# Kernel optimization log

Hardware: AMD Instinct MI355X
Metric: run time of the kernel (lower is better)

The kernel has to match this reference:

```python
import jax, jax.numpy as jnp
import numpy as np

H = 1024; NH = 16; L = 4; K = 128; N = 65536
ADIM_MOVE = 9; ADIM_TURN = 4; S = 2 * K + 2


def setup_inputs() -> dict:
    key = jax.random.key(0)
    ks = jax.random.split(key, 24)
    s = 0.02
    d = {}
    d['x'] = jax.random.normal(ks[0], (1, H), jnp.float32)
    d['memory_vectors'] = jax.random.normal(ks[1], (N, H), jnp.float32)
    d['memory_next_vectors'] = jax.random.normal(ks[2], (N, H), jnp.float32)
    d['memory_surprises'] = jax.random.uniform(ks[3], (N,), jnp.float32)
    d['memory_rewards'] = jax.random.normal(ks[4], (N,), jnp.float32)
    d['rand_noise'] = jax.random.uniform(ks[5], (N,), jnp.float32)
    d['action_idx_move'] = jax.random.randint(ks[6], (N,), 0, ADIM_MOVE)
    d['action_idx_turn'] = jax.random.randint(ks[7], (N,), 0, ADIM_TURN)
    d['start_token'] = jax.random.uniform(ks[8], (1, H)) * 2 - 1
    d['pos_emb'] = jax.random.uniform(ks[9], (S, H)) * 2 - 1
    d['in_proj_w'] = jax.random.normal(ks[10], (L, 3 * H, H)) * s
    d['in_proj_b'] = jnp.zeros((L, 3 * H))
    d['out_w'] = jax.random.normal(ks[11], (L, H, H)) * s
    d['out_b'] = jnp.zeros((L, H))
    d['ln1_w'] = jnp.ones((L, H)); d['ln1_b'] = jnp.zeros((L, H))
    d['ln2_w'] = jnp.ones((L, H)); d['ln2_b'] = jnp.zeros((L, H))
    d['ffn_w1'] = jax.random.normal(ks[12], (L, 4 * H, H)) * s
    d['ffn_b1'] = jnp.zeros((L, 4 * H))
    d['ffn_w2'] = jax.random.normal(ks[13], (L, H, 4 * H)) * s
    d['ffn_b2'] = jnp.zeros((L, H))
    d['act_move_w1'] = jax.random.normal(ks[14], (H, ADIM_MOVE)) * s
    d['act_move_b1'] = jnp.zeros((H,))
    d['act_move_w2'] = jax.random.normal(ks[15], (H, H)) * s
    d['act_move_b2'] = jnp.zeros((H,))
    d['act_turn_w1'] = jax.random.normal(ks[16], (H, ADIM_TURN)) * s
    d['act_turn_b1'] = jnp.zeros((H,))
    d['act_turn_w2'] = jax.random.normal(ks[17], (H, H)) * s
    d['act_turn_b2'] = jnp.zeros((H,))
    d['vh_w1'] = jax.random.normal(ks[18], (4 * H, H)) * s
    d['vh_b1'] = jnp.zeros((4 * H,))
    d['vh_w2'] = jax.random.normal(ks[19], (1, 4 * H)) * s
    d['vh_b2'] = jnp.zeros((1,))
    return d


def _get_scores(v):
    # tie-aware average rank / N (matches torch unique_consecutive logic)
    srt = jnp.sort(v)
    left = jnp.searchsorted(srt, v, side='left')
    right = jnp.searchsorted(srt, v, side='right')
    return ((left + right - 1).astype(v.dtype) / 2) / v.shape[0]


def _ln(x, w, b):
    m = x.mean(-1, keepdims=True)
    var = ((x - m) ** 2).mean(-1, keepdims=True)
    return (x - m) / jnp.sqrt(var + 1e-5) * w + b


def _gelu(x):
    return jax.nn.gelu(x, approximate=False)


def _mha(x, wqkv, bqkv, wo, bo, mask):
    dh = H // NH
    qkv = x @ wqkv.T + bqkv                      # [S, 3H]
    q, k, v = jnp.split(qkv, 3, axis=-1)
    q = q.reshape(-1, NH, dh); k = k.reshape(-1, NH, dh); v = v.reshape(-1, NH, dh)
    att = jnp.einsum('qhd,khd->hqk', q, k) / np.sqrt(dh).astype(np.float32)
    att = jax.nn.softmax(att + mask, axis=-1)
    o = jnp.einsum('hqk,khd->qhd', att, v).reshape(-1, H)
    return o @ wo.T + bo


def reference(x, memory_vectors, memory_next_vectors, memory_surprises, memory_rewards, rand_noise, action_idx_move, action_idx_turn, start_token, pos_emb, in_proj_w, in_proj_b, out_w, out_b, ln1_w, ln1_b, ln2_w, ln2_b, ffn_w1, ffn_b1, ffn_w2, ffn_b2, act_move_w1, act_move_b1, act_move_w2, act_move_b2, act_turn_w1, act_turn_b1, act_turn_w2, act_turn_b2, vh_w1, vh_b1, vh_w2, vh_b2):
    eps = 1e-8
    # ---- scoring (no_grad in original) ----
    xs = jax.lax.stop_gradient(x)
    xn = xs / jnp.maximum(jnp.linalg.norm(xs, axis=-1, keepdims=True), eps)
    mn = memory_vectors / jnp.maximum(jnp.linalg.norm(memory_vectors, axis=-1, keepdims=True), eps)
    sim = mn @ xn[0]                              # [N]
    scores = _get_scores(memory_surprises) ** 2 + _get_scores(sim) ** 2 + _get_scores(rand_noise) ** 2
    _, idx = jax.lax.top_k(scores, K)             # [K]
    # ---- gather memories + action one-hots ----
    sel = jax.lax.stop_gradient(memory_vectors[idx])   # [K, H]
    oh_move = jax.nn.one_hot(action_idx_move[idx], ADIM_MOVE, dtype=x.dtype)
    oh_turn = jax.nn.one_hot(action_idx_turn[idx], ADIM_TURN, dtype=x.dtype)
    av_move = _gelu(oh_move @ act_move_w1.T + act_move_b1) @ act_move_w2.T + act_move_b2
    av_turn = _gelu(oh_turn @ act_turn_w1.T + act_turn_b1) @ act_turn_w2.T + act_turn_b2
    av = (av_move + av_turn) / 2                  # mean over actions
    # interleave [v0, a0, v1, a1, ...], prepend start, append target
    vecs = jnp.stack((sel, av), axis=1).reshape(-1, H)
    vecs = jnp.concatenate((start_token, vecs, x), axis=0)   # [S, H]
    vecs = vecs + pos_emb
    mask = jnp.where(jnp.tril(jnp.ones((S, S), bool)), 0.0, -jnp.inf).astype(x.dtype)
    for l in range(L):
        vecs = vecs + _mha(_ln(vecs, ln1_w[l], ln1_b[l]), in_proj_w[l], in_proj_b[l], out_w[l], out_b[l], mask)
        h = _ln(vecs, ln2_w[l], ln2_b[l])
        vecs = vecs + _gelu(h @ ffn_w1[l].T + ffn_b1[l]) @ ffn_w2[l].T + ffn_b2[l]
    vidx = jnp.arange(K + 1) * 2 + 1
    vh_in = vecs[vidx]
    vp = _gelu(vh_in @ vh_w1.T + vh_b1) @ vh_w2.T + vh_b2   # [K+1, 1]
    sel_rewards = memory_rewards[idx]
    losses = (vp[:-1].ravel() - sel_rewards) ** 2            # mse, reduction='none'
    return (vecs[1:], memory_next_vectors[idx], vp[-1], losses, sel_rewards)
```

## Files before the change

### kernel.cpp

```cpp
#include <hip/hip_runtime.h>
#include <hip/hip_bf16.h>
#include <math.h>
#include <stdint.h>

typedef unsigned int u32;
typedef unsigned short u16;
typedef unsigned long long u64;

#define NM   65536
#define HD   1024
#define KS   128
#define SQ   258
#define NL   4
#define NBIN 65536
#define CCAP 2048

using bf16x8 = __attribute__((ext_vector_type(8))) short;
using f32x4v = __attribute__((ext_vector_type(4))) float;

static constexpr size_t A256(size_t x){ return (x + 255) & ~(size_t)255; }

constexpr size_t OFF_H3   = 0;
constexpr size_t OFF_C3   = OFF_H3 + (size_t)3*NBIN*4;
constexpr size_t OFF_HS   = OFF_C3 + (size_t)3*NBIN*4;
constexpr size_t ZERO_BYTES = OFF_HS + (size_t)NBIN*4;
constexpr u32 ZBLK = 1792;
constexpr size_t OFF_BS   = A256(ZERO_BYTES);
constexpr size_t OFF_P3   = A256(OFF_BS + 192*4);
constexpr size_t OFF_K3   = A256(OFF_P3 + (size_t)3*(NBIN+1)*4);
constexpr size_t OFF_L3   = A256(OFF_K3 + (size_t)3*NM*4);
constexpr size_t OFF_KSC  = A256(OFF_L3 + (size_t)3*NM*2);
constexpr size_t OFF_IDX  = A256(OFF_KSC + (size_t)NM*4);
constexpr size_t OFF_REW  = A256(OFF_IDX  + (size_t)KS*4);
constexpr size_t OFF_HM   = A256(OFF_REW  + (size_t)KS*4);
constexpr size_t OFF_HT   = A256(OFF_HM   + (size_t)KS*HD*2);
constexpr size_t OFF_VECS = A256(OFF_HT   + (size_t)KS*HD*2);
constexpr size_t OFF_LNB  = A256(OFF_VECS + (size_t)SQ*HD*4);
constexpr size_t OFF_QKV  = A256(OFF_LNB  + (size_t)SQ*HD*2);
constexpr size_t OFF_ATT  = A256(OFF_QKV  + (size_t)SQ*3*HD*2);
constexpr size_t OFF_FFH  = A256(OFF_ATT  + (size_t)SQ*HD*2);
constexpr size_t OFF_VHIN = A256(OFF_FFH  + (size_t)SQ*4*HD*2);
constexpr size_t OFF_WB   = A256(OFF_VHIN + (size_t)129*HD*2);
constexpr size_t NWELEM   = 56623104;
constexpr size_t OFF_PART = A256(OFF_WB + NWELEM*2);

constexpr size_t WB_IN = 0;
constexpr size_t WB_O  = WB_IN + (size_t)4*3*HD*HD;
constexpr size_t WB_F1 = WB_O  + (size_t)4*HD*HD;
constexpr size_t WB_F2 = WB_F1 + (size_t)4*4*HD*HD;
constexpr size_t WB_AM = WB_F2 + (size_t)4*4*HD*HD;
constexpr size_t WB_AT = WB_AM + (size_t)HD*HD;
constexpr size_t WB_VH = WB_AT + (size_t)HD*HD;

constexpr int OUT_NEXT = 257*HD;
constexpr int OUT_VP   = OUT_NEXT + KS*HD;
constexpr int OUT_LOSS = OUT_VP + 1;
constexpr int OUT_REWO = OUT_LOSS + KS;

__device__ __forceinline__ float gelu_f(float v){
  return 0.5f*v*(1.0f + erff(v*0.70710678118654752440f));
}

__device__ __forceinline__ u16 f2bf(float f){
  __hip_bfloat16 h = __float2bfloat16(f);
  u16 s; __builtin_memcpy(&s, &h, sizeof(u16));
  return s;
}

__device__ __forceinline__ float bf2f(u16 v){ return __uint_as_float(((u32)v) << 16); }

__device__ __forceinline__ float4 unpk4(u64 pk){
  u32 lo = (u32)pk, hi = (u32)(pk >> 32);
  float4 v;
  v.x = __uint_as_float(lo << 16);
  v.y = __uint_as_float(lo & 0xFFFF0000u);
  v.z = __uint_as_float(hi << 16);
  v.w = __uint_as_float(hi & 0xFFFF0000u);
  return v;
}

__device__ __forceinline__ u64 pk4(float4 v){
  u16 r[4] = { f2bf(v.x), f2bf(v.y), f2bf(v.z), f2bf(v.w) };
  u64 pk; __builtin_memcpy(&pk, r, 8);
  return pk;
}

__device__ __forceinline__ u32 fkey(float v){
  u32 b = __float_as_uint(v);
  return (b >> 31) ? ~b : (b | 0x80000000u);
}

__device__ __forceinline__ void gload16(const u16* g, u16* l){
  __builtin_amdgcn_global_load_lds(
      (const __attribute__((address_space(1))) unsigned int*)g,
      (__attribute__((address_space(3))) unsigned int*)l, 16, 0, 0);
}

struct WSeg { const float* s; u16* d; u32 base4, end4; };
struct WCA { WSeg seg[7]; u32 tot4; u32* z; };
__global__ __launch_bounds__(256) void k_wconv(WCA a){
  if(blockIdx.x < ZBLK) a.z[blockIdx.x*256 + threadIdx.x] = 0u;
  u32 i = blockIdx.x*256 + threadIdx.x;
  if(i >= a.tot4) return;
  #pragma unroll
  for(int j=0;j<7;++j){
    if(i < a.seg[j].end4){
      u32 off = i - a.seg[j].base4;
      float4 v = *(const float4*)&a.seg[j].s[(size_t)off*4];
      *(u64*)&a.seg[j].d[(size_t)off*4] = pk4(v);
      return;
    }
  }
}

__global__ __launch_bounds__(256) void k_simkey(const float* __restrict__ mv, const float* __restrict__ x,
                                                const float* __restrict__ surp, const float* __restrict__ noise,
                                                u32* __restrict__ keys3, u32* __restrict__ hist3){
  __shared__ float xs[HD];
  __shared__ float red[256];
  int t = threadIdx.x;
  float s = 0.f;
  for(int i=t;i<HD;i+=256){ float v=x[i]; s += v*v; }
  red[t]=s; __syncthreads();
  for(int o=128;o>0;o>>=1){ if(t<o) red[t]+=red[t+o]; __syncthreads(); }
  float nrm = fmaxf(sqrtf(red[0]), 1e-8f);
  for(int i=t;i<HD;i+=256) xs[i] = x[i]/nrm;
  __syncthreads();
  int lane = t & 63, w = t >> 6;
  #pragma unroll
  for(int rep=0;rep<2;++rep){
    int row = blockIdx.x*8 + rep*4 + w;
    const float4* p = (const float4*)(mv + (size_t)row*HD);
    const float4* q = (const float4*)xs;
    float d=0.f, ss=0.f;
    #pragma unroll
    for(int r=0;r<4;++r){
      float4 v = p[lane + 64*r]; float4 u = q[lane + 64*r];
      d  += v.x*u.x + v.y*u.y + v.z*u.z + v.w*u.w;
      ss += v.x*v.x + v.y*v.y + v.z*v.z + v.w*v.w;
    }
    for(int off=32;off>0;off>>=1){ d += __shfl_xor(d,off,64); ss += __shfl_xor(ss,off,64); }
    if(lane==0){
      float sim = d / fmaxf(sqrtf(ss),1e-8f);
      float vals[3] = { surp[row], sim, noise[row] };
      #pragma unroll
      for(int a=0;a<3;++a){
        u32 k = fkey(vals[a]);
        keys3[(size_t)a*NM + row] = k;
        atomicAdd(&hist3[(size_t)a*NBIN + (k >> 16)], 1u);
      }
    }
  }
}

__global__ __launch_bounds__(256) void k_scanA(const u32* __restrict__ hist3, u32* __restrict__ bsum){
  __shared__ u32 red[256];
  int blk = blockIdx.x;
  int t = threadIdx.x;
  const u32* h = hist3 + (size_t)(blk>>6)*NBIN + (size_t)(blk&63)*1024;
  u32 s = 0;
  #pragma unroll
  for(int j=0;j<4;++j) s += h[t*4+j];
  red[t]=s; __syncthreads();
  for(int o=128;o>0;o>>=1){ if(t<o) red[t]+=red[t+o]; __syncthreads(); }
  if(t==0) bsum[blk] = red[0];
}

__global__ __launch_bounds__(256) void k_scanC(const u32* __restrict__ hist3, const u32* __restrict__ bsum,
                                               u32* __restrict__ pref3){
  __shared__ u32 part[256];
  int blk = blockIdx.x;
  int t = threadIdx.x;
  int a = blk >> 6, c = blk & 63;
  u32 base = 0;
  for(int j=0;j<c;++j) base += bsum[a*64 + j];
  const u32* h = hist3 + (size_t)a*NBIN + (size_t)c*1024;
  u32* pref = pref3 + (size_t)a*(NBIN+1) + (size_t)c*1024;
  u32 loc[4]; u32 s = 0;
  #pragma unroll
  for(int j=0;j<4;++j){ loc[j] = h[t*4+j]; s += loc[j]; }
  part[t] = s; __syncthreads();
  for(int off=1;off<256;off<<=1){
    u32 u = (t >= off) ? part[t-off] : 0u;
    __syncthreads(); part[t] += u; __syncthreads();
  }
  u32 run = base + part[t] - s;
  #pragma unroll
  for(int j=0;j<4;++j){ pref[t*4+j] = run; run += loc[j]; }
  if(c == 63 && t == 255) pref3[(size_t)a*(NBIN+1) + NBIN] = NM;
}

__global__ void k_scatter3(const u32* __restrict__ keys3, const u32* __restrict__ pref3,
                           u32* __restrict__ cnt3, u16* __restrict__ lo3){
  int i = blockIdx.x*256 + threadIdx.x;
  if(i >= NM) return;
  #pragma unroll
  for(int a=0;a<3;++a){
    u32 k = keys3[(size_t)a*NM + i];
    u32 b = k >> 16;
    u32 pos = pref3[(size_t)a*(NBIN+1) + b] + atomicAdd(&cnt3[(size_t)a*NBIN + b], 1u);
    lo3[(size_t)a*NM + pos] = (u16)(k & 0xFFFFu);
  }
}

__global__ void k_rank3score(const u32* __restrict__ keys3, const u32* __restrict__ pref3,
                             const u16* __restrict__ lo3, u32* __restrict__ keysS, u32* __restrict__ histS){
  int i = blockIdx.x*256 + threadIdx.x;
  if(i >= NM) return;
  float rr[3];
  #pragma unroll
  for(int a=0;a<3;++a){
    u32 k = keys3[(size_t)a*NM + i];
    u32 b = k >> 16, my = k & 0xFFFFu;
    const u32* pref = pref3 + (size_t)a*(NBIN+1);
    const u16* lo = lo3 + (size_t)a*NM;
    u32 s = pref[b], e = pref[b+1];
    u32 nl = 0, ne = 0;
    for(u32 j=s;j<e;++j){ u32 u = lo[j]; nl += (u < my); ne += (u == my); }
    u32 left = s + nl, right = left + ne;
    rr[a] = (float)(left + right - 1) * (1.0f/131072.0f);
  }
  float sc = __fadd_rn(__fadd_rn(__fmul_rn(rr[0],rr[0]), __fmul_rn(rr[1],rr[1])), __fmul_rn(rr[2],rr[2]));
  u32 k = __float_as_uint(sc);
  keysS[i] = k;
  atomicAdd(&histS[k >> 16], 1u);
}

__global__ __launch_bounds__(1024) void k_selsort(const u32* __restrict__ histS, const u32* __restrict__ keysS,
                                                  int* __restrict__ idx){
  __shared__ u32 part[1024];
  __shared__ u64 sm[CCAP];
  __shared__ u32 thrT, cnt;
  int t = threadIdx.x;
  u32 base = t*64, s = 0;
  for(int j=0;j<64;++j) s += histS[base+j];
  part[t] = s; __syncthreads();
  for(int off=1;off<1024;off<<=1){
    u32 v = (t+off < 1024) ? part[t+off] : 0u;
    __syncthreads(); part[t] += v; __syncthreads();
  }
  u32 above = part[t] - s;
  if(above < (u32)KS && above + s >= (u32)KS){
    u32 cum = above;
    for(int j=63;j>=0;--j){
      u32 c = histS[base+j];
      if(cum + c >= (u32)KS){ thrT = (u32)(base+j) << 16; cnt = 0; break; }
      cum += c;
    }
  }
  __syncthreads();
  u32 T = thrT;
  for(int i=t;i<NM;i+=1024){
    u32 k = keysS[i];
    if(k >= T){
      u32 p = atomicAdd(&cnt, 1u);
      if(p < (u32)CCAP) sm[p] = ((u64)(~k) << 32) | (u32)i;
    }
  }
  __syncthreads();
  u32 n = cnt; if(n > (u32)CCAP) n = CCAP;
  for(int i=t;i<CCAP;i+=1024) if(i >= (int)n) sm[i] = 0xFFFFFFFFFFFFFFFFull;
  __syncthreads();
  for(int k=2;k<=CCAP;k<<=1){
    for(int j=k>>1;j>0;j>>=1){
      for(int i=t;i<CCAP;i+=1024){
        int ixj = i ^ j;
        if(ixj > i){
          bool up = ((i & k) == 0);
          u64 a = sm[i], b = sm[ixj];
          if((a > b) == up){ sm[i] = b; sm[ixj] = a; }
        }
      }
      __syncthreads();
    }
  }
  if(t < KS) idx[t] = (int)(sm[t] & 0xFFFFFFFFu);
}

__global__ void k_gather(const int* __restrict__ idx,
                         const float* __restrict__ mv, const float* __restrict__ mnv,
                         const float* __restrict__ mrew,
                         const int* __restrict__ aim, const int* __restrict__ ait,
                         const float* __restrict__ amw1, const float* __restrict__ amb1,
                         const float* __restrict__ atw1, const float* __restrict__ atb1,
                         const float* __restrict__ start, const float* __restrict__ x,
                         const float* __restrict__ pos,
                         float* __restrict__ vecs, float* __restrict__ outnext,
                         u16* __restrict__ hm, u16* __restrict__ ht,
                         float* __restrict__ rew, float* __restrict__ outrew){
  int k = blockIdx.x;
  int t = threadIdx.x;
  if(k < KS){
    int row = idx[k];
    const float4* a = (const float4*)(mv  + (size_t)row*HD);
    const float4* b = (const float4*)(mnv + (size_t)row*HD);
    const float4* pz = (const float4*)(pos + (size_t)(2*k+1)*HD);
    float4* vr = (float4*)(vecs + (size_t)(2*k+1)*HD);
    float4* on = (float4*)(outnext + (size_t)k*HD);
    float4 av = a[t], bv = b[t], pv = pz[t];
    av.x += pv.x; av.y += pv.y; av.z += pv.z; av.w += pv.w;
    vr[t] = av; on[t] = bv;
    int am = aim[row], at = ait[row];
    for(int j=t;j<HD;j+=256){
      hm[(size_t)k*HD+j] = f2bf(gelu_f(amw1[(size_t)j*9 + am] + amb1[j]));
      ht[(size_t)k*HD+j] = f2bf(gelu_f(atw1[(size_t)j*4 + at] + atb1[j]));
    }
    if(t == 0){ float r = mrew[row]; rew[k] = r; outrew[k] = r; }
  } else {
    const float4* st = (const float4*)start;
    const float4* xx = (const float4*)x;
    const float4* p0 = (const float4*)pos;
    const float4* p1 = (const float4*)(pos + (size_t)(SQ-1)*HD);
    float4 v0 = st[t], v1 = xx[t], q0 = p0[t], q1 = p1[t];
    v0.x += q0.x; v0.y += q0.y; v0.z += q0.z; v0.w += q0.w;
    v1.x += q1.x; v1.y += q1.y; v1.z += q1.z; v1.w += q1.w;
    ((float4*)vecs)[t] = v0;
    ((float4*)(vecs + (size_t)(SQ-1)*HD))[t] = v1;
  }
}

__device__ __forceinline__ void gemm_body(u16* As, u16* Bs, const u16* __restrict__ A, const u16* __restrict__ B,
        u16* __restrict__ P, int M, int N, int K, int S, int nbm, int lda, int tile){
  int bm = (tile % nbm) * 64;
  int tmp = tile / nbm;
  int z  = tmp % S;
  int bn = (tmp / S) * 64;
  int Ks = K / S, kbeg = z*Ks;
  int nk = Ks >> 6;

  int t = threadIdx.x, lane = t & 63, w = t >> 6;
  int s0 = w*64 + lane, s1 = s0 + 256;
  int r0s = s0 >> 3, c0s = (s0 & 7) ^ (r0s & 7);
  int r1s = s1 >> 3, c1s = (s1 & 7) ^ (r1s & 7);
  const u16* ga0 = A + (size_t)(bm + r0s)*lda + kbeg + c0s*8;
  const u16* ga1 = A + (size_t)(bm + r1s)*lda + kbeg + c1s*8;
  const u16* gb0 = B + (size_t)(bn + r0s)*K  + kbeg + c0s*8;
  const u16* gb1 = B + (size_t)(bn + r1s)*K  + kbeg + c1s*8;
  int lb0 = w*512, lb1 = 2048 + w*512;

  int wm = (w >> 1)*32, wn = (w & 1)*32;
  int lr = lane & 15, lg = lane >> 4;
  int ra0 = wm + lr, ra1 = ra0 + 16;
  int rb0 = wn + lr, rb1 = rb0 + 16;
  int a00 = ra0*64 + ((lg     ^ (ra0&7))*8);
  int a01 = ra0*64 + (((4+lg) ^ (ra0&7))*8);
  int a10 = ra1*64 + ((lg     ^ (ra1&7))*8);
  int a11 = ra1*64 + (((4+lg) ^ (ra1&7))*8);
  int b00 = rb0*64 + ((lg     ^ (rb0&7))*8);
  int b01 = rb0*64 + (((4+lg) ^ (rb0&7))*8);
  int b10 = rb1*64 + ((lg     ^ (rb1&7))*8);
  int b11 = rb1*64 + (((4+lg) ^ (rb1&7))*8);

  f32x4v acc00 = {0,0,0,0}, acc01 = {0,0,0,0}, acc10 = {0,0,0,0}, acc11 = {0,0,0,0};

  gload16(ga0, As + lb0); gload16(ga1, As + lb1);
  gload16(gb0, Bs + lb0); gload16(gb1, Bs + lb1);
  ga0 += 64; ga1 += 64; gb0 += 64; gb1 += 64;
  __syncthreads();

  for(int kk = 0; kk < nk; ++kk){
    int cur = (kk & 1) << 12;
    if(kk + 1 < nk){
      int nxt = cur ^ 4096;
      gload16(ga0, As + nxt + lb0); gload16(ga1, As + nxt + lb1);
      gload16(gb0, Bs + nxt + lb0); gload16(gb1, Bs + nxt + lb1);
      ga0 += 64; ga1 += 64; gb0 += 64; gb1 += 64;
    }
    bf16x8 xa0 = *(const bf16x8*)&As[cur + a00];
    bf16x8 xa1 = *(const bf16x8*)&As[cur + a10];
    bf16x8 xb0 = *(const bf16x8*)&Bs[cur + b00];
    bf16x8 xb1 = *(const bf16x8*)&Bs[cur + b10];
    acc00 = __builtin_amdgcn_mfma_f32_16x16x32_bf16(xa0, xb0, acc00, 0, 0, 0);
    acc01 = __builtin_amdgcn_mfma_f32_16x16x32_bf16(xa0, xb1, acc01, 0, 0, 0);
    acc10 = __builtin_amdgcn_mfma_f32_16x16x32_bf16(xa1, xb0, acc10, 0, 0, 0);
    acc11 = __builtin_amdgcn_mfma_f32_16x16x32_bf16(xa1, xb1, acc11, 0, 0, 0);
    xa0 = *(const bf16x8*)&As[cur + a01];
    xa1 = *(const bf16x8*)&As[cur + a11];
    xb0 = *(const bf16x8*)&Bs[cur + b01];
    xb1 = *(const bf16x8*)&Bs[cur + b11];
    acc00 = __builtin_amdgcn_mfma_f32_16x16x32_bf16(xa0, xb0, acc00, 0, 0, 0);
    acc01 = __builtin_amdgcn_mfma_f32_16x16x32_bf16(xa0, xb1, acc01, 0, 0, 0);
    acc10 = __builtin_amdgcn_mfma_f32_16x16x32_bf16(xa1, xb0, acc10, 0, 0, 0);
    acc11 = __builtin_amdgcn_mfma_f32_16x16x32_bf16(xa1, xb1, acc11, 0, 0, 0);
    __syncthreads();
  }

  size_t zbase = (size_t)z * (size_t)M;
  #pragma unroll
  for(int r=0;r<4;++r){
    int row0 = bm + wm + lg*4 + r;
    int row1 = row0 + 16;
    int cc0 = bn + wn + lr, cc1 = cc0 + 16;
    if(row0 < M){
      P[(zbase+row0)*N + cc0] = f2bf(acc00[r]);
      P[(zbase+row0)*N + cc1] = f2bf(acc01[r]);
    }
    if(row1 < M){
      P[(zbase+row1)*N + cc0] = f2bf(acc10[r]);
      P[(zbase+row1)*N + cc1] = f2bf(acc11[r]);
    }
  }
}

__global__ __launch_bounds__(256) void k_gemm(const u16* __restrict__ A, const u16* __restrict__ B,
        u16* __restrict__ P, int M, int N, int K, int S, int nbm, int lda){
  __shared__ u16 As[8192];
  __shared__ u16 Bs[8192];
  u32 nwg = gridDim.x, orig = blockIdx.x;
  u32 swz = (orig & 7)*(nwg >> 3) + (orig >> 3);
  gemm_body(As, Bs, A, B, P, M, N, K, S, nbm, lda, (int)swz);
}

__global__ __launch_bounds__(256) void k_actgemm(const u16* __restrict__ hm, const u16* __restrict__ ht,
        const u16* __restrict__ amw2, const u16* __restrict__ atw2,
        u16* __restrict__ part, u16* __restrict__ part2){
  __shared__ u16 As[8192];
  __shared__ u16 Bs[8192];
  int which = blockIdx.x >> 8, tile = blockIdx.x & 255;
  gemm_body(As, Bs, which ? ht : hm, which ? atw2 : amw2, which ? part2 : part,
            KS, HD, HD, 8, 2, HD, tile);
}

template<int S_, int ACT, bool BFOUT>
__global__ __launch_bounds__(256) void k_finS(const u16* __restrict__ P, const float* __restrict__ bias,
                                              float* __restrict__ C, u16* __restrict__ Cb, int MN4, int Nd){
  int i4 = blockIdx.x*256 + threadIdx.x;
  if(i4 >= MN4) return;
  size_t off = (size_t)i4*4;
  size_t MN = (size_t)MN4*4;
  float4 v = unpk4(*(const u64*)&P[off]);
  #pragma unroll
  for(int z=1;z<S_;++z){
    float4 q = unpk4(*(const u64*)&P[(size_t)z*MN + off]);
    v.x += q.x; v.y += q.y; v.z += q.z; v.w += q.w;
  }
  int j = (i4 % (Nd/4))*4;
  float4 b4 = *(const float4*)&bias[j];
  v.x += b4.x; v.y += b4.y; v.z += b4.z; v.w += b4.w;
  if(ACT == 1){ v.x = gelu_f(v.x); v.y = gelu_f(v.y); v.z = gelu_f(v.z); v.w = gelu_f(v.w); }
  if(BFOUT) *(u64*)&Cb[off] = pk4(v);
  else      *(float4*)&C[off] = v;
}

template<int S_, bool LN>
__global__ __launch_bounds__(256) void k_finrow(const u16* __restrict__ P, const float* __restrict__ bias,
                                                float* __restrict__ vecs, const float* __restrict__ lw,
                                                const float* __restrict__ lb, u16* __restrict__ lnb,
                                                float* __restrict__ outp, u16* __restrict__ vhin){
  __shared__ float red[256];
  int row = blockIdx.x, t = threadIdx.x;
  int j = t*4;
  float4 v = unpk4(*(const u64*)&P[(size_t)row*HD + j]);
  #pragma unroll
  for(int z=1;z<S_;++z){
    float4 p = unpk4(*(const u64*)&P[((size_t)z*SQ + row)*HD + j]);
    v.x += p.x; v.y += p.y; v.z += p.z; v.w += p.w;
  }
  float4 b4 = *(const float4*)&bias[j];
  float4 r4 = *(const float4*)&vecs[(size_t)row*HD + j];
  v.x += b4.x + r4.x; v.y += b4.y + r4.y; v.z += b4.z + r4.z; v.w += b4.w + r4.w;
  *(float4*)&vecs[(size_t)row*HD + j] = v;
  if(LN){
    red[t] = v.x+v.y+v.z+v.w; __syncthreads();
    for(int o=128;o>0;o>>=1){ if(t<o) red[t]+=red[t+o]; __syncthreads(); }
    float m = red[0]*(1.0f/HD); __syncthreads();
    float dx=v.x-m, dy=v.y-m, dz=v.z-m, dw=v.w-m;
    red[t] = dx*dx+dy*dy+dz*dz+dw*dw; __syncthreads();
    for(int o=128;o>0;o>>=1){ if(t<o) red[t]+=red[t+o]; __syncthreads(); }
    float den = sqrtf(red[0]*(1.0f/HD) + 1e-5f);
    float4 w4 = *(const float4*)&lw[j];
    float4 lb4 = *(const float4*)&lb[j];
    float4 o4;
    o4.x = dx/den*w4.x + lb4.x; o4.y = dy/den*w4.y + lb4.y;
    o4.z = dz/den*w4.z + lb4.z; o4.w = dw/den*w4.w + lb4.w;
    *(u64*)&lnb[(size_t)row*HD + j] = pk4(o4);
  } else {
    if(row >= 1) *(float4*)&outp[(size_t)(row-1)*HD + j] = v;
    if(row & 1){
      int vr = (row-1) >> 1;
      *(u64*)&vhin[(size_t)vr*HD + j] = pk4(v);
    }
  }
}

__global__ __launch_bounds__(256) void k_finavln(const u16* __restrict__ Pm, const u16* __restrict__ Pt,
                                                 const float* __restrict__ bm_, const float* __restrict__ bt_,
                                                 const float* __restrict__ pos, float* __restrict__ vecs,
                                                 const float* __restrict__ lw, const float* __restrict__ lb,
                                                 u16* __restrict__ lnb){
  __shared__ float red[256];
  int row = blockIdx.x, t = threadIdx.x;
  int j = t*4;
  float4 v;
  if(row >= 2 && row <= 256 && ((row & 1) == 0)){
    int k = (row-2) >> 1;
    float4 s = {0,0,0,0};
    #pragma unroll
    for(int z=0;z<8;++z){
      float4 a = unpk4(*(const u64*)&Pm[((size_t)z*KS + k)*HD + j]);
      float4 b = unpk4(*(const u64*)&Pt[((size_t)z*KS + k)*HD + j]);
      s.x += a.x+b.x; s.y += a.y+b.y; s.z += a.z+b.z; s.w += a.w+b.w;
    }
    float4 bm4 = *(const float4*)&bm_[j];
    float4 bt4 = *(const float4*)&bt_[j];
    float4 p4 = *(const float4*)&pos[(size_t)row*HD + j];
    v.x = 0.5f*(s.x + bm4.x + bt4.x) + p4.x;
    v.y = 0.5f*(s.y + bm4.y + bt4.y) + p4.y;
    v.z = 0.5f*(s.z + bm4.z + bt4.z) + p4.z;
    v.w = 0.5f*(s.w + bm4.w + bt4.w) + p4.w;
    *(float4*)&vecs[(size_t)row*HD + j] = v;
  } else {
    v = *(const float4*)&vecs[(size_t)row*HD + j];
  }
  red[t] = v.x+v.y+v.z+v.w; __syncthreads();
  for(int o=128;o>0;o>>=1){ if(t<o) red[t]+=red[t+o]; __syncthreads(); }
  float m = red[0]*(1.0f/HD); __syncthreads();
  float dx=v.x-m, dy=v.y-m, dz=v.z-m, dw=v.w-m;
  red[t] = dx*dx+dy*dy+dz*dz+dw*dw; __syncthreads();
  for(int o=128;o>0;o>>=1){ if(t<o) red[t]+=red[t+o]; __syncthreads(); }
  float den = sqrtf(red[0]*(1.0f/HD) + 1e-5f);
  float4 w4 = *(const float4*)&lw[j];
  float4 lb4 = *(const float4*)&lb[j];
  float4 o4;
  o4.x = dx/den*w4.x + lb4.x; o4.y = dy/den*w4.y + lb4.y;
  o4.z = dz/den*w4.z + lb4.z; o4.w = dw/den*w4.w + lb4.w;
  *(u64*)&lnb[(size_t)row*HD + j] = pk4(o4);
}

__global__ void k_attn(const u16* __restrict__ qkv, u16* __restrict__ outp){
  __shared__ float qv[64];
  __shared__ float p[SQ];
  __shared__ float red[256];
  int h = blockIdx.y, t = threadIdx.x;
  #pragma unroll
  for(int half=0; half<2; ++half){
    int q = half ? (SQ-1 - (int)blockIdx.x) : (int)blockIdx.x;
    if(t < 64) qv[t] = bf2f(qkv[(size_t)q*3072 + h*64 + t]);
    __syncthreads();
    int nk = q + 1;
    float lmax = -1e30f;
    for(int j=t;j<nk;j+=256){
      const u32* kr = (const u32*)(qkv + (size_t)j*3072 + 1024 + h*64);
      float d = 0.f;
      #pragma unroll
      for(int c2=0;c2<32;++c2){
        u32 pk = kr[c2];
        d += qv[c2*2]   * __uint_as_float(pk << 16);
        d += qv[c2*2+1] * __uint_as_float(pk & 0xFFFF0000u);
      }
      d *= 0.125f;
      p[j] = d;
      lmax = fmaxf(lmax, d);
    }
    red[t] = lmax; __syncthreads();
    for(int o=128;o>0;o>>=1){ if(t<o) red[t] = fmaxf(red[t], red[t+o]); __syncthreads(); }
    float m = red[0];
    __syncthreads();
    float lsum = 0.f;
    for(int j=t;j<nk;j+=256){ float e = expf(p[j]-m); p[j] = e; lsum += e; }
    red[t] = lsum; __syncthreads();
    for(int o=128;o>0;o>>=1){ if(t<o) red[t] += red[t+o]; __syncthreads(); }
    float inv = 1.0f/red[0];
    __syncthreads();
    int d = t & 63, g = t >> 6;
    float acc = 0.f;
    for(int j=g;j<nk;j+=4) acc += p[j]*bf2f(qkv[(size_t)j*3072 + 2048 + h*64 + d]);
    red[t] = acc; __syncthreads();
    if(g == 0){
      float o4 = red[d] + red[64+d] + red[128+d] + red[192+d];
      outp[(size_t)q*HD + h*64 + d] = f2bf(o4*inv);
    }
    __syncthreads();
  }
}

__global__ __launch_bounds__(256) void k_vpfin(const u16* __restrict__ P, const float* __restrict__ vb1,
                                               const float* __restrict__ vw2, const float* __restrict__ vb2,
                                               const float* __restrict__ rew, float* __restrict__ outp){
  __shared__ float red[256];
  int r = blockIdx.x, t = threadIdx.x;
  float s = 0.f;
  for(int c4=t;c4<1024;c4+=256){
    float4 v = unpk4(*(const u64*)&P[(size_t)r*4096 + c4*4]);
    #pragma unroll
    for(int z=1;z<4;++z){
      float4 q = unpk4(*(const u64*)&P[((size_t)z*129 + r)*4096 + c4*4]);
      v.x += q.x; v.y += q.y; v.z += q.z; v.w += q.w;
    }
    float4 b4 = *(const float4*)&vb1[c4*4];
    float4 w4 = *(const float4*)&vw2[c4*4];
    s += gelu_f(v.x + b4.x)*w4.x + gelu_f(v.y + b4.y)*w4.y
       + gelu_f(v.z + b4.z)*w4.z + gelu_f(v.w + b4.w)*w4.w;
  }
  red[t]=s; __syncthreads();
  for(int o=128;o>0;o>>=1){ if(t<o) red[t]+=red[t+o]; __syncthreads(); }
  if(t == 0){
    float val = red[0] + vb2[0];
    if(r == KS) outp[OUT_VP] = val;
    else { float d = val - rew[r]; outp[OUT_LOSS + r] = d*d; }
  }
}

extern "C" void kernel_launch(void* const* d_in, const int* in_sizes, int n_in,
                              void* d_out, int out_size, void* d_ws, size_t ws_size,
                              hipStream_t stream){
  const float* x     = (const float*)d_in[0];
  const float* mv    = (const float*)d_in[1];
  const float* mnv   = (const float*)d_in[2];
  const float* surp  = (const float*)d_in[3];
  const float* mrew  = (const float*)d_in[4];
  const float* noise = (const float*)d_in[5];
  const int*   aim   = (const int*)d_in[6];
  const int*   ait   = (const int*)d_in[7];
  const float* start = (const float*)d_in[8];
  const float* pos   = (const float*)d_in[9];
  const float* inW = (const float*)d_in[10]; const float* inB = (const float*)d_in[11];
  const float* oW  = (const float*)d_in[12]; const float* oB  = (const float*)d_in[13];
  const float* l1w = (const float*)d_in[14]; const float* l1b = (const float*)d_in[15];
  const float* l2w = (const float*)d_in[16]; const float* l2b = (const float*)d_in[17];
  const float* f1w = (const float*)d_in[18]; const float* f1b = (const float*)d_in[19];
  const float* f2w = (const float*)d_in[20]; const float* f2b = (const float*)d_in[21];
  const float* amw1= (const float*)d_in[22]; const float* amb1= (const float*)d_in[23];
  const float* amw2= (const float*)d_in[24]; const float* amb2= (const float*)d_in[25];
  const float* atw1= (const float*)d_in[26]; const float* atb1= (const float*)d_in[27];
  const float* atw2= (const float*)d_in[28]; const float* atb2= (const float*)d_in[29];
  const float* vw1 = (const float*)d_in[30]; const float* vb1 = (const float*)d_in[31];
  const float* vw2 = (const float*)d_in[32]; const float* vb2 = (const float*)d_in[33];

  float* out = (float*)d_out;
  char* ws = (char*)d_ws;
  u32*  hist3 = (u32*)(ws+OFF_H3);
  u32*  cnt3  = (u32*)(ws+OFF_C3);
  u32*  histS = (u32*)(ws+OFF_HS);
  u32*  bsum  = (u32*)(ws+OFF_BS);
  u32*  pref3 = (u32*)(ws+OFF_P3);
  u32*  keys3 = (u32*)(ws+OFF_K3);
  u16*  lo3   = (u16*)(ws+OFF_L3);
  u32*  keysS = (u32*)(ws+OFF_KSC);
  int*  idxb  = (int*)(ws+OFF_IDX);
  float* rew  = (float*)(ws+OFF_REW);
  u16*  hm    = (u16*)(ws+OFF_HM);
  u16*  ht    = (u16*)(ws+OFF_HT);
  float* vecs = (float*)(ws+OFF_VECS);
  u16*  lnb   = (u16*)(ws+OFF_LNB);
  u16*  qkvb  = (u16*)(ws+OFF_QKV);
  u16*  attn  = (u16*)(ws+OFF_ATT);
  u16*  ffh   = (u16*)(ws+OFF_FFH);
  u16*  vhin  = (u16*)(ws+OFF_VHIN);
  u16*  wb    = (u16*)(ws+OFF_WB);
  u16*  part  = (u16*)(ws+OFF_PART);
  u16*  part2 = part + (size_t)8*KS*HD;

  u16* inW_bf = wb + WB_IN;
  u16* oW_bf  = wb + WB_O;
  u16* f1w_bf = wb + WB_F1;
  u16* f2w_bf = wb + WB_F2;
  u16* am_bf  = wb + WB_AM;
  u16* at_bf  = wb + WB_AT;
  u16* vh_bf  = wb + WB_VH;

  dim3 b256(256);
  int gN = NM/256;

  {
    WCA a;
    const float* srcs[7] = { inW, oW, f1w, f2w, amw2, atw2, vw1 };
    u16* dsts[7] = { inW_bf, oW_bf, f1w_bf, f2w_bf, am_bf, at_bf, vh_bf };
    u32 sizes4[7] = { 4*3*HD*HD/4, 4*HD*HD/4, 4*4*HD*HD/4, 4*4*HD*HD/4, HD*HD/4, HD*HD/4, 4*HD*HD/4 };
    u32 cum = 0;
    for(int j=0;j<7;++j){
      a.seg[j].s = srcs[j]; a.seg[j].d = dsts[j];
      a.seg[j].base4 = cum; cum += sizes4[j]; a.seg[j].end4 = cum;
    }
    a.tot4 = cum;
    a.z = (u32*)ws;
    hipLaunchKernelGGL(k_wconv, dim3((cum + 255)/256), b256, 0, stream, a);
  }

  hipLaunchKernelGGL(k_simkey, dim3(NM/8), b256, 0, stream, mv, x, surp, noise, keys3, hist3);
  hipLaunchKernelGGL(k_scanA, dim3(192), b256, 0, stream, hist3, bsum);
  hipLaunchKernelGGL(k_scanC, dim3(192), b256, 0, stream, hist3, bsum, pref3);
  hipLaunchKernelGGL(k_scatter3, dim3(gN), b256, 0, stream, keys3, pref3, cnt3, lo3);
  hipLaunchKernelGGL(k_rank3score, dim3(gN), b256, 0, stream, keys3, pref3, lo3, keysS, histS);
  hipLaunchKernelGGL(k_selsort, dim3(1), dim3(1024), 0, stream, histS, keysS, idxb);

  hipLaunchKernelGGL(k_gather, dim3(KS+1), b256, 0, stream, idxb, mv, mnv, mrew, aim, ait,
                     amw1, amb1, atw1, atb1, start, x, pos,
                     vecs, out + OUT_NEXT, hm, ht, rew, out + OUT_REWO);
  hipLaunchKernelGGL(k_actgemm, dim3(512), b256, 0, stream, hm, ht, am_bf, at_bf, part, part2);
  hipLaunchKernelGGL(k_finavln, dim3(SQ), b256, 0, stream, part, part2, amb2, atb2, pos, vecs, l1w, l1b, lnb);

  for(int l=0;l<NL;++l){
    hipLaunchKernelGGL(k_gemm, dim3(960), b256, 0, stream, lnb, inW_bf + (size_t)l*3*HD*HD, part, SQ, 3*HD, HD, 4, 5, HD);
    hipLaunchKernelGGL((k_finS<4,0,true>), dim3(774), b256, 0, stream, part, inB + (size_t)l*3*HD, (float*)nullptr, qkvb, SQ*3*HD/4, 3*HD);
    hipLaunchKernelGGL(k_attn, dim3(SQ/2, 16), b256, 0, stream, qkvb, attn);
    hipLaunchKernelGGL(k_gemm, dim3(640), b256, 0, stream, attn, oW_bf + (size_t)l*HD*HD, part, SQ, HD, HD, 8, 5, HD);
    hipLaunchKernelGGL((k_finrow<8,true>), dim3(SQ), b256, 0, stream, part, oB + (size_t)l*HD, vecs,
                       l2w + (size_t)l*HD, l2b + (size_t)l*HD, lnb, (float*)nullptr, (u16*)nullptr);
    hipLaunchKernelGGL(k_gemm, dim3(1280), b256, 0, stream, lnb, f1w_bf + (size_t)l*4*HD*HD, part, SQ, 4*HD, HD, 4, 5, HD);
    hipLaunchKernelGGL((k_finS<4,1,true>), dim3(1032), b256, 0, stream, part, f1b + (size_t)l*4*HD, (float*)nullptr, ffh, SQ*4*HD/4, 4*HD);
    hipLaunchKernelGGL(k_gemm, dim3(640), b256, 0, stream, ffh, f2w_bf + (size_t)l*HD*4*HD, part, SQ, HD, 4*HD, 8, 5, 4*HD);
    if(l < NL-1)
      hipLaunchKernelGGL((k_finrow<8,true>), dim3(SQ), b256, 0, stream, part, f2b + (size_t)l*HD, vecs,
                         l1w + (size_t)(l+1)*HD, l1b + (size_t)(l+1)*HD, lnb, (float*)nullptr, (u16*)nullptr);
    else
      hipLaunchKernelGGL((k_finrow<8,false>), dim3(SQ), b256, 0, stream, part, f2b + (size_t)l*HD, vecs,
                         (const float*)nullptr, (const float*)nullptr, (u16*)nullptr, out, vhin);
  }

  hipLaunchKernelGGL(k_gemm, dim3(768), b256, 0, stream, vhin, vh_bf, part, KS+1, 4*HD, HD, 4, 3, HD);
  hipLaunchKernelGGL(k_vpfin, dim3(KS+1), b256, 0, stream, part, vb1, vw2, vb2, rew, out);
}
```

Measured before the change: 825.7 us.

## Fuse split-K reduction and bias/GELU epilogue into GEMM via last-block counters

```diff
diff --git a/kernel.cpp b/kernel.cpp
--- a/kernel.cpp
+++ b/kernel.cpp
@@ -23,8 +23,9 @@
 constexpr size_t OFF_H3   = 0;
 constexpr size_t OFF_C3   = OFF_H3 + (size_t)3*NBIN*4;
 constexpr size_t OFF_HS   = OFF_C3 + (size_t)3*NBIN*4;
-constexpr size_t ZERO_BYTES = OFF_HS + (size_t)NBIN*4;
-constexpr u32 ZBLK = 1792;
+constexpr size_t OFF_CTR  = OFF_HS + (size_t)NBIN*4;
+constexpr size_t ZERO_BYTES = OFF_CTR + 16384;
+constexpr u32 ZBLK = 1808;
 constexpr size_t OFF_BS   = A256(ZERO_BYTES);
 constexpr size_t OFF_P3   = A256(OFF_BS + 192*4);
 constexpr size_t OFF_K3   = A256(OFF_P3 + (size_t)3*(NBIN+1)*4);
@@ -411,6 +412,50 @@
   gemm_body(As, Bs, A, B, P, M, N, K, S, nbm, lda, (int)swz);
 }
 
+template<int S_, int ACT>
+__global__ __launch_bounds__(256) void k_gemmF(const u16* __restrict__ A, const u16* __restrict__ B,
+        u16* __restrict__ P, const float* __restrict__ bias, u16* __restrict__ Cb,
+        u32* __restrict__ ctr, int M, int N, int K, int nbm, int lda){
+  __shared__ u16 As[8192];
+  __shared__ u16 Bs[8192];
+  __shared__ u32 lastflag;
+  u32 nwg = gridDim.x, orig = blockIdx.x;
+  u32 swz = (orig & 7)*(nwg >> 3) + (orig >> 3);
+  gemm_body(As, Bs, A, B, P, M, N, K, S_, nbm, lda, (int)swz);
+  int tile = (int)swz;
+  int bmi = tile % nbm;
+  int tmp = tile / nbm;
+  int bni = tmp / S_;
+  int nbn = N >> 6;
+  __threadfence();
+  __syncthreads();
+  if(threadIdx.x == 0){
+    u32 old = atomicAdd(&ctr[bmi*nbn + bni], 1u);
+    lastflag = (old == (u32)(S_-1)) ? 1u : 0u;
+  }
+  __syncthreads();
+  if(lastflag){
+    __threadfence();
+    int bm = bmi*64, bn = bni*64;
+    for(int idx = threadIdx.x; idx < 1024; idx += 256){
+      int rl = idx >> 4, cg = idx & 15;
+      int row = bm + rl;
+      if(row >= M) continue;
+      int col = bn + cg*4;
+      float4 v = unpk4(*(const u64*)&P[(size_t)row*N + col]);
+      #pragma unroll
+      for(int z=1; z<S_; ++z){
+        float4 q = unpk4(*(const u64*)&P[((size_t)z*M + row)*N + col]);
+        v.x += q.x; v.y += q.y; v.z += q.z; v.w += q.w;
+      }
+      float4 b4 = *(const float4*)&bias[col];
+      v.x += b4.x; v.y += b4.y; v.z += b4.z; v.w += b4.w;
+      if(ACT == 1){ v.x = gelu_f(v.x); v.y = gelu_f(v.y); v.z = gelu_f(v.z); v.w = gelu_f(v.w); }
+      *(u64*)&Cb[(size_t)row*N + col] = pk4(v);
+    }
+  }
+}
+
 __global__ __launch_bounds__(256) void k_actgemm(const u16* __restrict__ hm, const u16* __restrict__ ht,
         const u16* __restrict__ amw2, const u16* __restrict__ atw2,
         u16* __restrict__ part, u16* __restrict__ part2){
@@ -419,27 +464,6 @@
   int which = blockIdx.x >> 8, tile = blockIdx.x & 255;
   gemm_body(As, Bs, which ? ht : hm, which ? atw2 : amw2, which ? part2 : part,
             KS, HD, HD, 8, 2, HD, tile);
-}
-
-template<int S_, int ACT, bool BFOUT>
-__global__ __launch_bounds__(256) void k_finS(const u16* __restrict__ P, const float* __restrict__ bias,
-                                              float* __restrict__ C, u16* __restrict__ Cb, int MN4, int Nd){
-  int i4 = blockIdx.x*256 + threadIdx.x;
-  if(i4 >= MN4) return;
-  size_t off = (size_t)i4*4;
-  size_t MN = (size_t)MN4*4;
-  float4 v = unpk4(*(const u64*)&P[off]);
-  #pragma unroll
-  for(int z=1;z<S_;++z){
-    float4 q = unpk4(*(const u64*)&P[(size_t)z*MN + off]);
-    v.x += q.x; v.y += q.y; v.z += q.z; v.w += q.w;
-  }
-  int j = (i4 % (Nd/4))*4;
-  float4 b4 = *(const float4*)&bias[j];
-  v.x += b4.x; v.y += b4.y; v.z += b4.z; v.w += b4.w;
-  if(ACT == 1){ v.x = gelu_f(v.x); v.y = gelu_f(v.y); v.z = gelu_f(v.z); v.w = gelu_f(v.w); }
-  if(BFOUT) *(u64*)&Cb[off] = pk4(v);
-  else      *(float4*)&C[off] = v;
 }
 
 template<int S_, bool LN>
@@ -632,6 +656,7 @@
   u32*  hist3 = (u32*)(ws+OFF_H3);
   u32*  cnt3  = (u32*)(ws+OFF_C3);
   u32*  histS = (u32*)(ws+OFF_HS);
+  u32*  tctr  = (u32*)(ws+OFF_CTR);
   u32*  bsum  = (u32*)(ws+OFF_BS);
   u32*  pref3 = (u32*)(ws+OFF_P3);
   u32*  keys3 = (u32*)(ws+OFF_K3);
@@ -691,14 +716,14 @@
   hipLaunchKernelGGL(k_finavln, dim3(SQ), b256, 0, stream, part, part2, amb2, atb2, pos, vecs, l1w, l1b, lnb);
 
   for(int l=0;l<NL;++l){
-    hipLaunchKernelGGL(k_gemm, dim3(960), b256, 0, stream, lnb, inW_bf + (size_t)l*3*HD*HD, part, SQ, 3*HD, HD, 4, 5, HD);
-    hipLaunchKernelGGL((k_finS<4,0,true>), dim3(774), b256, 0, stream, part, inB + (size_t)l*3*HD, (float*)nullptr, qkvb, SQ*3*HD/4, 3*HD);
+    hipLaunchKernelGGL((k_gemmF<4,0>), dim3(960), b256, 0, stream, lnb, inW_bf + (size_t)l*3*HD*HD,
+                       part, inB + (size_t)l*3*HD, qkvb, tctr + (size_t)l*1024, SQ, 3*HD, HD, 5, HD);
     hipLaunchKernelGGL(k_attn, dim3(SQ/2, 16), b256, 0, stream, qkvb, attn);
     hipLaunchKernelGGL(k_gemm, dim3(640), b256, 0, stream, attn, oW_bf + (size_t)l*HD*HD, part, SQ, HD, HD, 8, 5, HD);
     hipLaunchKernelGGL((k_finrow<8,true>), dim3(SQ), b256, 0, stream, part, oB + (size_t)l*HD, vecs,
                        l2w + (size_t)l*HD, l2b + (size_t)l*HD, lnb, (float*)nullptr, (u16*)nullptr);
-    hipLaunchKernelGGL(k_gemm, dim3(1280), b256, 0, stream, lnb, f1w_bf + (size_t)l*4*HD*HD, part, SQ, 4*HD, HD, 4, 5, HD);
-    hipLaunchKernelGGL((k_finS<4,1,true>), dim3(1032), b256, 0, stream, part, f1b + (size_t)l*4*HD, (float*)nullptr, ffh, SQ*4*HD/4, 4*HD);
+    hipLaunchKernelGGL((k_gemmF<4,1>), dim3(1280), b256, 0, stream, lnb, f1w_bf + (size_t)l*4*HD*HD,
+                       part, f1b + (size_t)l*4*HD, ffh, tctr + (size_t)l*1024 + 512, SQ, 4*HD, HD, 5, HD);
     hipLaunchKernelGGL(k_gemm, dim3(640), b256, 0, stream, ffh, f2w_bf + (size_t)l*HD*4*HD, part, SQ, HD, 4*HD, 8, 5, 4*HD);
     if(l < NL-1)
       hipLaunchKernelGGL((k_finrow<8,true>), dim3(SQ), b256, 0, stream, part, f2b + (size_t)l*HD, vecs,
```

Measured after the change: 2.177 ms. 164% more time.
